# Kernel tuning notes

Hardware: AMD Instinct MI355X
Metric: run time of the kernel (lower is better)

Reference implementation:

```python
import jax, jax.numpy as jnp
import numpy as np

N_NEURON = 1024
N_PEPTIDE = 16
N_GENES = 1
BATCH = 2048
SQ = 32  # int(sqrt(N_NEURON))
DT = 1.0 / 120.0
STATE_SIZE = N_NEURON + N_GENES + N_NEURON + N_NEURON * N_PEPTIDE  # 18433


def setup_inputs() -> dict:
    key = jax.random.key(0)
    ks = jax.random.split(key, 10)
    # structured state: [ablate_mat | pc2 | neuron | peptide]
    ablate_mat = jnp.ones((BATCH, N_NEURON), jnp.float32)
    pc2 = jax.random.uniform(ks[0], (BATCH, N_GENES), jnp.float32)
    neuron = jax.random.normal(ks[1], (BATCH, N_NEURON), jnp.float32)
    peptide = jax.random.uniform(ks[2], (BATCH, N_NEURON * N_PEPTIDE), jnp.float32)
    state = jnp.concatenate([ablate_mat, pc2, neuron, peptide], axis=-1)
    u = jax.random.normal(ks[3], (BATCH, 1), jnp.float32)
    # uniform noise sample used by the exp firing noise; keep strictly < 1
    noise_u = jax.random.uniform(ks[4], (BATCH, N_NEURON), jnp.float32, 1e-6, 1.0 - 1e-6)
    D = jax.random.uniform(ks[5], (N_PEPTIDE,), jnp.float32)
    pep_prod_rate = jax.random.uniform(ks[6], (N_PEPTIDE,), jnp.float32)
    pep_decay_rate = jax.random.uniform(ks[7], (N_PEPTIDE,), jnp.float32)
    pep_action = jax.random.normal(ks[8], (N_PEPTIDE,), jnp.float32)
    synapse_matrix = jax.random.normal(ks[9], (N_NEURON, N_NEURON), jnp.float32) * 0.02
    neuron_decay = jnp.ones((1,), jnp.float32) * 0.5
    input_layer = jax.random.normal(jax.random.fold_in(key, 11), (N_NEURON,), jnp.float32)
    return dict(u=u, state=state, noise_u=noise_u, D=D, pep_prod_rate=pep_prod_rate,
                pep_decay_rate=pep_decay_rate, pep_action=pep_action,
                synapse_matrix=synapse_matrix, neuron_decay=neuron_decay,
                input_layer=input_layer)


def reference(u, state, noise_u, D, pep_prod_rate, pep_decay_rate, pep_action,
              synapse_matrix, neuron_decay, input_layer):
    # func = abs (log_train=False)
    Dp = jnp.abs(D)
    prod_r = jnp.abs(pep_prod_rate)
    decay_r = jnp.abs(pep_decay_rate)
    ndecay = jnp.abs(neuron_decay)

    # unpack state: [ablate | pc2 | neuron | peptide]
    ablate_mat = state[:, :N_NEURON]
    pc2 = state[:, N_NEURON:N_NEURON + N_GENES]
    neuron = state[:, N_NEURON + N_GENES:2 * N_NEURON + N_GENES]
    pep_flat = state[:, 2 * N_NEURON + N_GENES:]
    peptide = pep_flat.reshape(-1, N_NEURON, N_PEPTIDE)

    firing = jax.nn.relu(neuron) * ablate_mat
    neuron = neuron * ablate_mat

    # noisy_fire, noise='exp': firing = -(firing+0.01)*log(1-U)
    firing = -(firing + 0.01) * jnp.log1p(-noise_u)
    firing = jnp.clip(firing, 0.0, 10.0)

    # peptide production / decay
    pep_prod = prod_r * firing[:, :, None]           # (b, n, p)
    pep_decay = decay_r * peptide                    # (b, n, p)

    # wrap-around 2D Laplacian diffusion stencil on (SQ, SQ) grid
    ps = peptide.reshape(-1, SQ, SQ, N_PEPTIDE)
    lap = (jnp.roll(ps, -1, axis=1) + jnp.roll(ps, 1, axis=1)
           + jnp.roll(ps, -1, axis=2) + jnp.roll(ps, 1, axis=2) - 4.0 * ps)
    pep_diffuse = (Dp * lap).reshape(-1, N_NEURON, N_PEPTIDE)

    # neuron dynamics
    d_neuron = jnp.sum(peptide * pep_action, axis=-1) * pc2
    d_neuron = d_neuron + firing @ synapse_matrix
    d_neuron = d_neuron - neuron * ndecay
    d_neuron = d_neuron + input_layer * u            # (b,1)*(n,) broadcast

    d_peptide = (pep_prod - pep_decay + pep_diffuse).reshape(-1, N_NEURON * N_PEPTIDE)
    pep_new = pep_flat + d_peptide * DT
    neuron_new = (neuron + d_neuron * DT) * ablate_mat

    state_new = jnp.concatenate([ablate_mat, pc2, neuron_new, pep_new], axis=-1)
    # return_firing=True
    return firing, state_new
```

## Files before the change

### kernel.cpp

```cpp
#include <hip/hip_runtime.h>
#include <hip/hip_bf16.h>

#define N_NEURON 1024
#define N_PEPTIDE 16
#define N_GENES 1
#define BATCH 2048
#define SQ 32
#define DT_STEP (1.0f/120.0f)
#define S_STRIDE (N_NEURON + N_GENES + N_NEURON + N_NEURON*N_PEPTIDE)

typedef __attribute__((ext_vector_type(8))) short short8;
typedef __attribute__((ext_vector_type(4))) float floatx4;
typedef __attribute__((ext_vector_type(2))) float floatx2;
typedef floatx4 floatx4u __attribute__((aligned(4)));
typedef floatx2 floatx2u __attribute__((aligned(4)));

__global__ __launch_bounds__(256) void synT_cast(const float* __restrict__ syn,
                                                 __hip_bfloat16* __restrict__ synT) {
    __shared__ float tile[32][33];
    const int n0 = blockIdx.x * 32;
    const int k0 = blockIdx.y * 32;
    const int tx = threadIdx.x & 31;
    const int ty = threadIdx.x >> 5;
    #pragma unroll
    for (int i = 0; i < 4; ++i)
        tile[ty + i*8][tx] = syn[(long)(k0 + ty + i*8) * N_NEURON + n0 + tx];
    __syncthreads();
    #pragma unroll
    for (int i = 0; i < 4; ++i)
        synT[(long)(n0 + ty + i*8) * N_NEURON + k0 + tx] =
            __float2bfloat16(tile[tx][ty + i*8]);
}

__global__ __launch_bounds__(256) void pep_fused(
    const float* __restrict__ u,
    const float* __restrict__ state,
    const float* __restrict__ noise,
    const float* __restrict__ D,
    const float* __restrict__ prod_g,
    const float* __restrict__ decay_g,
    const float* __restrict__ pact_g,
    const float* __restrict__ ndecay_g,
    const float* __restrict__ inL,
    float* __restrict__ firing_out,
    float* __restrict__ state_new,
    __hip_bfloat16* __restrict__ fbf)
{
    __shared__ floatx4 slab4[18 * 128];
    __shared__ float sf[512];
    __shared__ float sn[512];
    __shared__ float sps[512];

    const int b   = blockIdx.x >> 1;
    const int h   = blockIdx.x & 1;
    const int tid = threadIdx.x;
    const long bS = (long)b * S_STRIDE;
    const int r0  = h * 16;
    const float u_b  = u[b];
    const float pc2  = state[bS + N_NEURON];
    const float ndecay = fabsf(ndecay_g[0]);

    const float* __restrict__ pep = state + bS + 2 * N_NEURON + N_GENES;
    float* __restrict__ pep_new = state_new + bS + 2 * N_NEURON + N_GENES;

    floatx4 sl[8];
    #pragma unroll
    for (int k = 0; k < 8; ++k)
        sl[k] = *(const floatx4u*)(pep + r0 * 512 + (tid + k * 256) * 4);
    floatx4 halo;
    {
        const int hr = (tid < 128) ? ((r0 + 31) & 31) : ((r0 + 16) & 31);
        const int ht = tid & 127;
        halo = *(const floatx4u*)(pep + hr * 512 + ht * 4);
    }

    const int gn = h * 512 + tid * 2;
    floatx2 abv = *(const floatx2u*)(state + bS + gn);
    floatx2 nrv = *(const floatx2u*)(state + bS + N_NEURON + N_GENES + gn);
    floatx2 nzv = *(const floatx2*)(noise + (long)b * N_NEURON + gn);

    #pragma unroll
    for (int k = 0; k < 8; ++k)
        slab4[128 + tid + k * 256] = sl[k];
    if (tid < 128) slab4[tid] = halo;
    else           slab4[2176 + tid - 128] = halo;

    {
        floatx2 fv, nmv;
        #pragma unroll
        for (int j = 0; j < 2; ++j) {
            nmv[j] = nrv[j] * abv[j];
            float fr = fmaxf(nrv[j], 0.f) * abv[j];
            fr = -(fr + 0.01f) * log1pf(-nzv[j]);
            fr = fminf(fmaxf(fr, 0.f), 10.f);
            fv[j] = fr;
        }
        *(floatx2*)(firing_out + (long)b * N_NEURON + gn) = fv;
        __hip_bfloat16 h0 = __float2bfloat16(fv[0]);
        __hip_bfloat16 h1 = __float2bfloat16(fv[1]);
        unsigned int packed = (unsigned int)(*(unsigned short*)&h0) |
                              ((unsigned int)(*(unsigned short*)&h1) << 16);
        *(unsigned int*)(fbf + (long)b * N_NEURON + gn) = packed;
        *(floatx2u*)(state_new + bS + gn) = abv;
        *(floatx2*)(sf + tid * 2) = fv;
        *(floatx2*)(sn + tid * 2) = nmv;
    }
    if (h == 0 && tid == 0) state_new[bS + N_NEURON] = pc2;
    __syncthreads();

    const int pq = tid & 3;
    const int nl = tid >> 2;
    const int p0q = pq * 4;
    floatx4 Dq, prq, deq, paq;
    #pragma unroll
    for (int j = 0; j < 4; ++j) {
        Dq[j]  = fabsf(D[p0q + j]);
        prq[j] = fabsf(prod_g[p0q + j]);
        deq[j] = fabsf(decay_g[p0q + j]);
        paq[j] = pact_g[p0q + j];
    }

    #pragma unroll 2
    for (int it = 0; it < 8; ++it) {
        const int n_l  = it * 64 + nl;
        const int si_l = (n_l >> 5) + 1;
        const int sj   = n_l & 31;
        const floatx4 c  = slab4[(si_l * 32 + sj) * 4 + pq];
        const floatx4 vu = slab4[((si_l - 1) * 32 + sj) * 4 + pq];
        const floatx4 vd = slab4[((si_l + 1) * 32 + sj) * 4 + pq];
        const floatx4 vl = slab4[(si_l * 32 + ((sj + 31) & 31)) * 4 + pq];
        const floatx4 vr = slab4[(si_l * 32 + ((sj + 1) & 31)) * 4 + pq];
        const float fn = sf[n_l];
        floatx4 lap = vu + vd + vl + vr - 4.f * c;
        floatx4 outv = c + DT_STEP * (prq * fn - deq * c + Dq * lap);
        *(floatx4u*)(pep_new + ((h * 512 + n_l) << 4) + p0q) = outv;

        float ps = c[0]*paq[0] + c[1]*paq[1] + c[2]*paq[2] + c[3]*paq[3];
        ps += __shfl_xor(ps, 1);
        ps += __shfl_xor(ps, 2);
        if (pq == 0) sps[n_l] = ps;
    }
    __syncthreads();

    {
        const int n2  = tid * 2;
        const int gn2 = h * 512 + n2;
        floatx2 ss = *(const floatx2*)(sps + n2);
        floatx2 nm = *(const floatx2*)(sn + n2);
        floatx2 il = *(const floatx2*)(inL + gn2);
        floatx2 c0;
        #pragma unroll
        for (int j = 0; j < 2; ++j)
            c0[j] = nm[j] + DT_STEP * (ss[j] * pc2 - nm[j] * ndecay + il[j] * u_b);
        *(floatx2u*)(state_new + bS + N_NEURON + N_GENES + gn2) = c0;
    }
}

__device__ __forceinline__ void stage8k(const __hip_bfloat16* __restrict__ gbase,
                                        char* lhalf, int row0, int k0,
                                        int w, int lane)
{
    #pragma unroll
    for (int i = 0; i < 2; ++i) {
        const int ch  = w * 2 + i;
        const int o   = ch * 1024 + lane * 16;
        const int row = o >> 7;
        const int c16 = (o >> 4) & 7;
        const int cl  = c16 ^ (row & 7);
        const __hip_bfloat16* g = gbase + (long)(row0 + row) * 1024 + k0 + cl * 8;
        __builtin_amdgcn_global_load_lds(
            (const __attribute__((address_space(1))) void*)g,
            (__attribute__((address_space(3))) void*)(lhalf + ch * 1024),
            16, 0, 0);
    }
}

__device__ __forceinline__ short8 lds_frag(const char* lhalf, int row, int c16) {
    const int cl = c16 ^ (row & 7);
    return *(const short8*)(lhalf + row * 128 + cl * 16);
}

__global__ __launch_bounds__(256) void gemm_epi(
    const __hip_bfloat16* __restrict__ A,
    const __hip_bfloat16* __restrict__ BT,
    const float* __restrict__ state,
    float* __restrict__ state_new)
{
    __shared__ __align__(16) char lds[2][16384];
    const int tid = threadIdx.x;
    const int w = tid >> 6, lane = tid & 63;
    const int q = lane >> 4, l16 = lane & 15;
    const int m0 = blockIdx.x * 64;
    const int n0 = blockIdx.y * 64;
    const int wm = (w & 1) * 32, wn = (w >> 1) * 32;

    float abv[2][2][4], c0v[2][2][4];
    #pragma unroll
    for (int mi = 0; mi < 2; ++mi)
    #pragma unroll
    for (int ni = 0; ni < 2; ++ni)
    #pragma unroll
    for (int r = 0; r < 4; ++r) {
        const int m = m0 + wm + mi * 16 + q * 4 + r;
        const int n = n0 + wn + ni * 16 + l16;
        const long sidx = (long)m * S_STRIDE;
        abv[mi][ni][r] = state[sidx + n];
        c0v[mi][ni][r] = state_new[sidx + N_NEURON + N_GENES + n];
    }

    floatx4 acc[2][2] = {};

    stage8k(A,  lds[0],        m0, 0, w, lane);
    stage8k(BT, lds[0] + 8192, n0, 0, w, lane);
    __syncthreads();

#define GEMM_STEP(CUR, T)                                                     \
    {                                                                         \
        if ((T) < 15) {                                                       \
            stage8k(A,  lds[(CUR) ^ 1],        m0, ((T) + 1) * 64, w, lane);  \
            stage8k(BT, lds[(CUR) ^ 1] + 8192, n0, ((T) + 1) * 64, w, lane);  \
        }                                                                     \
        const char* la = lds[(CUR)];                                          \
        const char* lb = lds[(CUR)] + 8192;                                   \
        _Pragma("unroll")                                                     \
        for (int kk = 0; kk < 2; ++kk) {                                      \
            const int c16 = kk * 4 + q;                                       \
            short8 a0 = lds_frag(la, wm + l16,      c16);                     \
            short8 a1 = lds_frag(la, wm + 16 + l16, c16);                     \
            short8 b0 = lds_frag(lb, wn + l16,      c16);                     \
            short8 b1 = lds_frag(lb, wn + 16 + l16, c16);                     \
            acc[0][0] = __builtin_amdgcn_mfma_f32_16x16x32_bf16(a0, b0, acc[0][0], 0, 0, 0); \
            acc[0][1] = __builtin_amdgcn_mfma_f32_16x16x32_bf16(a0, b1, acc[0][1], 0, 0, 0); \
            acc[1][0] = __builtin_amdgcn_mfma_f32_16x16x32_bf16(a1, b0, acc[1][0], 0, 0, 0); \
            acc[1][1] = __builtin_amdgcn_mfma_f32_16x16x32_bf16(a1, b1, acc[1][1], 0, 0, 0); \
        }                                                                     \
        if ((T) < 15) __syncthreads();                                        \
    }

    #pragma unroll
    for (int tt = 0; tt < 8; ++tt) {
        GEMM_STEP(0, tt * 2)
        GEMM_STEP(1, tt * 2 + 1)
    }
#undef GEMM_STEP

    #pragma unroll
    for (int mi = 0; mi < 2; ++mi)
    #pragma unroll
    for (int ni = 0; ni < 2; ++ni)
    #pragma unroll
    for (int r = 0; r < 4; ++r) {
        const int m = m0 + wm + mi * 16 + q * 4 + r;
        const int n = n0 + wn + ni * 16 + l16;
        const long sidx = (long)m * S_STRIDE;
        state_new[sidx + N_NEURON + N_GENES + n] =
            (c0v[mi][ni][r] + DT_STEP * acc[mi][ni][r]) * abv[mi][ni][r];
    }
}

extern "C" void kernel_launch(void* const* d_in, const int* in_sizes, int n_in,
                              void* d_out, int out_size, void* d_ws, size_t ws_size,
                              hipStream_t stream) {
    const float* u      = (const float*)d_in[0];
    const float* state  = (const float*)d_in[1];
    const float* noise  = (const float*)d_in[2];
    const float* D      = (const float*)d_in[3];
    const float* prod   = (const float*)d_in[4];
    const float* decay  = (const float*)d_in[5];
    const float* pact   = (const float*)d_in[6];
    const float* syn    = (const float*)d_in[7];
    const float* ndec   = (const float*)d_in[8];
    const float* inL    = (const float*)d_in[9];

    float* firing = (float*)d_out;
    float* state_new = firing + (long)BATCH * N_NEURON;

    __hip_bfloat16* fbf  = (__hip_bfloat16*)d_ws;
    __hip_bfloat16* synT = fbf + (long)BATCH * N_NEURON;

    hipLaunchKernelGGL(synT_cast, dim3(32, 32), dim3(256), 0, stream, syn, synT);
    hipLaunchKernelGGL(pep_fused, dim3(BATCH * 2), dim3(256), 0, stream,
                       u, state, noise, D, prod, decay, pact, ndec, inL,
                       firing, state_new, fbf);
    hipLaunchKernelGGL(gemm_epi, dim3(32, 16), dim3(256), 0, stream,
                       fbf, synT, state, state_new);
}
```

Baseline: 316.2 us.

## Process whole batch row per block, drop halo, use nontemporal stores

The peptide kernel now launches one 512-thread block per batch row instead of two half-row blocks. The full 32x32 grid sits in shared memory, so the wrap-around halo rows no longer need to be reloaded, and each centre value is kept in registers for the stencil. The peptide-action dot product is computed before the first barrier, and the large output streams use nontemporal stores. In exchange, each block needs about 76KB of LDS and twice as many threads, which limits how many blocks fit on a CU at once.

```diff
diff --git a/kernel.cpp b/kernel.cpp
--- a/kernel.cpp
+++ b/kernel.cpp
@@ -32,7 +32,7 @@
             __float2bfloat16(tile[tx][ty + i*8]);
 }
 
-__global__ __launch_bounds__(256) void pep_fused(
+__global__ __launch_bounds__(512) void pep_fused(
     const float* __restrict__ u,
     const float* __restrict__ state,
     const float* __restrict__ noise,
@@ -46,16 +46,14 @@
     float* __restrict__ state_new,
     __hip_bfloat16* __restrict__ fbf)
 {
-    __shared__ floatx4 slab4[18 * 128];
-    __shared__ float sf[512];
-    __shared__ float sn[512];
-    __shared__ float sps[512];
-
-    const int b   = blockIdx.x >> 1;
-    const int h   = blockIdx.x & 1;
+    __shared__ floatx4 slab4[4096];
+    __shared__ float sf[N_NEURON];
+    __shared__ float sn[N_NEURON];
+    __shared__ float sps[N_NEURON];
+
+    const int b   = blockIdx.x;
     const int tid = threadIdx.x;
     const long bS = (long)b * S_STRIDE;
-    const int r0  = h * 16;
     const float u_b  = u[b];
     const float pc2  = state[bS + N_NEURON];
     const float ndecay = fabsf(ndecay_g[0]);
@@ -63,27 +61,40 @@
     const float* __restrict__ pep = state + bS + 2 * N_NEURON + N_GENES;
     float* __restrict__ pep_new = state_new + bS + 2 * N_NEURON + N_GENES;
 
+    const int pq = tid & 3;
+    const int nl = tid >> 2;
+    const int p0q = pq * 4;
+    floatx4 Dq, prq, deq, paq;
+    #pragma unroll
+    for (int j = 0; j < 4; ++j) {
+        Dq[j]  = fabsf(D[p0q + j]);
+        prq[j] = fabsf(prod_g[p0q + j]);
+        deq[j] = fabsf(decay_g[p0q + j]);
+        paq[j] = pact_g[p0q + j];
+    }
+
     floatx4 sl[8];
     #pragma unroll
     for (int k = 0; k < 8; ++k)
-        sl[k] = *(const floatx4u*)(pep + r0 * 512 + (tid + k * 256) * 4);
-    floatx4 halo;
-    {
-        const int hr = (tid < 128) ? ((r0 + 31) & 31) : ((r0 + 16) & 31);
-        const int ht = tid & 127;
-        halo = *(const floatx4u*)(pep + hr * 512 + ht * 4);
-    }
-
-    const int gn = h * 512 + tid * 2;
+        sl[k] = *(const floatx4u*)(pep + (tid + k * 512) * 4);
+
+    const int gn = tid * 2;
     floatx2 abv = *(const floatx2u*)(state + bS + gn);
     floatx2 nrv = *(const floatx2u*)(state + bS + N_NEURON + N_GENES + gn);
     floatx2 nzv = *(const floatx2*)(noise + (long)b * N_NEURON + gn);
 
     #pragma unroll
     for (int k = 0; k < 8; ++k)
-        slab4[128 + tid + k * 256] = sl[k];
-    if (tid < 128) slab4[tid] = halo;
-    else           slab4[2176 + tid - 128] = halo;
+        slab4[tid + k * 512] = sl[k];
+
+    #pragma unroll
+    for (int k = 0; k < 8; ++k) {
+        const int n = k * 128 + nl;
+        float ps = sl[k][0]*paq[0] + sl[k][1]*paq[1] + sl[k][2]*paq[2] + sl[k][3]*paq[3];
+        ps += __shfl_xor(ps, 1);
+        ps += __shfl_xor(ps, 2);
+        if (pq == 0) sps[n] = ps;
+    }
 
     {
         floatx2 fv, nmv;
@@ -95,64 +106,44 @@
             fr = fminf(fmaxf(fr, 0.f), 10.f);
             fv[j] = fr;
         }
-        *(floatx2*)(firing_out + (long)b * N_NEURON + gn) = fv;
+        __builtin_nontemporal_store(fv, (floatx2*)(firing_out + (long)b * N_NEURON + gn));
         __hip_bfloat16 h0 = __float2bfloat16(fv[0]);
         __hip_bfloat16 h1 = __float2bfloat16(fv[1]);
         unsigned int packed = (unsigned int)(*(unsigned short*)&h0) |
                               ((unsigned int)(*(unsigned short*)&h1) << 16);
         *(unsigned int*)(fbf + (long)b * N_NEURON + gn) = packed;
-        *(floatx2u*)(state_new + bS + gn) = abv;
-        *(floatx2*)(sf + tid * 2) = fv;
-        *(floatx2*)(sn + tid * 2) = nmv;
-    }
-    if (h == 0 && tid == 0) state_new[bS + N_NEURON] = pc2;
-    __syncthreads();
-
-    const int pq = tid & 3;
-    const int nl = tid >> 2;
-    const int p0q = pq * 4;
-    floatx4 Dq, prq, deq, paq;
-    #pragma unroll
-    for (int j = 0; j < 4; ++j) {
-        Dq[j]  = fabsf(D[p0q + j]);
-        prq[j] = fabsf(prod_g[p0q + j]);
-        deq[j] = fabsf(decay_g[p0q + j]);
-        paq[j] = pact_g[p0q + j];
-    }
-
-    #pragma unroll 2
+        __builtin_nontemporal_store(abv, (floatx2u*)(state_new + bS + gn));
+        *(floatx2*)(sf + gn) = fv;
+        *(floatx2*)(sn + gn) = nmv;
+    }
+    if (tid == 0) state_new[bS + N_NEURON] = pc2;
+    __syncthreads();
+
+    #pragma unroll
     for (int it = 0; it < 8; ++it) {
-        const int n_l  = it * 64 + nl;
-        const int si_l = (n_l >> 5) + 1;
-        const int sj   = n_l & 31;
-        const floatx4 c  = slab4[(si_l * 32 + sj) * 4 + pq];
-        const floatx4 vu = slab4[((si_l - 1) * 32 + sj) * 4 + pq];
-        const floatx4 vd = slab4[((si_l + 1) * 32 + sj) * 4 + pq];
-        const floatx4 vl = slab4[(si_l * 32 + ((sj + 31) & 31)) * 4 + pq];
-        const floatx4 vr = slab4[(si_l * 32 + ((sj + 1) & 31)) * 4 + pq];
-        const float fn = sf[n_l];
+        const int n  = it * 128 + nl;
+        const int si = n >> 5, sj = n & 31;
+        const floatx4 c  = sl[it];
+        const floatx4 vu = slab4[((((si + 31) & 31) * 32) + sj) * 4 + pq];
+        const floatx4 vd = slab4[((((si +  1) & 31) * 32) + sj) * 4 + pq];
+        const floatx4 vl = slab4[((si * 32) + ((sj + 31) & 31)) * 4 + pq];
+        const floatx4 vr = slab4[((si * 32) + ((sj +  1) & 31)) * 4 + pq];
+        const float fn = sf[n];
         floatx4 lap = vu + vd + vl + vr - 4.f * c;
         floatx4 outv = c + DT_STEP * (prq * fn - deq * c + Dq * lap);
-        *(floatx4u*)(pep_new + ((h * 512 + n_l) << 4) + p0q) = outv;
-
-        float ps = c[0]*paq[0] + c[1]*paq[1] + c[2]*paq[2] + c[3]*paq[3];
-        ps += __shfl_xor(ps, 1);
-        ps += __shfl_xor(ps, 2);
-        if (pq == 0) sps[n_l] = ps;
+        __builtin_nontemporal_store(outv, (floatx4u*)(pep_new + (n << 4) + p0q));
     }
     __syncthreads();
 
     {
-        const int n2  = tid * 2;
-        const int gn2 = h * 512 + n2;
-        floatx2 ss = *(const floatx2*)(sps + n2);
-        floatx2 nm = *(const floatx2*)(sn + n2);
-        floatx2 il = *(const floatx2*)(inL + gn2);
+        floatx2 ss = *(const floatx2*)(sps + gn);
+        floatx2 nm = *(const floatx2*)(sn + gn);
+        floatx2 il = *(const floatx2*)(inL + gn);
         floatx2 c0;
         #pragma unroll
         for (int j = 0; j < 2; ++j)
             c0[j] = nm[j] + DT_STEP * (ss[j] * pc2 - nm[j] * ndecay + il[j] * u_b);
-        *(floatx2u*)(state_new + bS + N_NEURON + N_GENES + gn2) = c0;
+        *(floatx2u*)(state_new + bS + N_NEURON + N_GENES + gn) = c0;
     }
 }
 
@@ -279,7 +270,7 @@
     __hip_bfloat16* synT = fbf + (long)BATCH * N_NEURON;
 
     hipLaunchKernelGGL(synT_cast, dim3(32, 32), dim3(256), 0, stream, syn, synT);
-    hipLaunchKernelGGL(pep_fused, dim3(BATCH * 2), dim3(256), 0, stream,
+    hipLaunchKernelGGL(pep_fused, dim3(BATCH), dim3(512), 0, stream,
                        u, state, noise, D, prod, decay, pact, ndec, inL,
                        firing, state_new, fbf);
     hipLaunchKernelGGL(gemm_epi, dim3(32, 16), dim3(256), 0, stream,
```

Result: no change. 316.1 us (-0.0%).
